# Performance work log

Measured on AMD Instinct MI355X. Metric: run time of the kernel, lower is better.

Reference implementation:

```python
import jax, jax.numpy as jnp
import numpy as np


def setup_inputs() -> dict:
    key = jax.random.key(0)
    ks = jax.random.split(key, 6)
    B, N, F, H, E = 2, 50000, 64, 32, 800000
    x = jax.random.normal(ks[0], (B, N, F), dtype=jnp.float32)
    edge_index = jax.random.randint(ks[1], (2, E), 0, N, dtype=jnp.int64)
    h_cur = jax.random.normal(ks[2], (B, N, H), dtype=jnp.float32)
    c_cur = jax.random.normal(ks[3], (B, N, H), dtype=jnp.float32)
    W = jax.random.normal(ks[4], (F + H, 4 * H), dtype=jnp.float32) * (1.0 / np.sqrt(F + H))
    b = jax.random.normal(ks[5], (4 * H,), dtype=jnp.float32) * 0.01
    return {"x": x, "edge_index": edge_index, "h_cur": h_cur, "c_cur": c_cur, "W": W, "b": b}


def reference(x, edge_index, h_cur, c_cur, W, b):
    B, N, _ = x.shape
    H = h_cur.shape[-1]

    # --- GCNConv on concatenated [x, h] ---
    combined = jnp.concatenate([x, h_cur], axis=-1)          # [B, N, F+H]
    xw = jnp.einsum('bnf,fg->bng', combined, W)              # [B, N, 4H]

    # add self-loops
    loop = jnp.arange(N, dtype=edge_index.dtype)
    src = jnp.concatenate([edge_index[0], loop])             # [E+N]
    dst = jnp.concatenate([edge_index[1], loop])             # [E+N]

    # symmetric degree normalization: deg over target index (PyG gcn_norm)
    deg = jnp.zeros((N,), dtype=xw.dtype).at[dst].add(1.0)
    dinv = jnp.where(deg > 0, jax.lax.rsqrt(deg), 0.0)
    norm = dinv[src] * dinv[dst]                             # [E+N]

    # gather-scale-scatter aggregation
    msgs = xw[:, src, :] * norm[None, :, None]               # [B, E+N, 4H]
    agg = jnp.zeros((B, N, 4 * H), dtype=xw.dtype).at[:, dst, :].add(msgs)
    conv = agg + b                                           # [B, N, 4H]

    # --- LSTM gating ---
    cc_i, cc_f, cc_o, cc_g = jnp.split(conv, 4, axis=-1)
    i = jax.nn.sigmoid(cc_i)
    f = jax.nn.sigmoid(cc_f)
    o = jax.nn.sigmoid(cc_o)
    g = jnp.tanh(cc_g)
    c_next = f * c_cur + i * g
    h_next = o * jnp.tanh(c_next)
    return h_next, c_next
```

## Files before the change

### kernel.cpp

```cpp
#include <hip/hip_runtime.h>
#include <hip/hip_bf16.h>

constexpr int H_DIM = 32;
constexpr int KPAD  = 104;
constexpr int CAP   = 64;
constexpr int PCAP  = 5120;
constexpr int EPB   = 2048;

typedef __attribute__((ext_vector_type(8))) short bf16x8;
typedef __attribute__((ext_vector_type(4))) float f32x4;

static __device__ __forceinline__ unsigned short f2bf_bits(float v) {
    __hip_bfloat16 b = __float2bfloat16(v);
    return *reinterpret_cast<unsigned short*>(&b);
}
static __device__ __forceinline__ unsigned pack2(float a, float b) {
    return (unsigned)f2bf_bits(a) | ((unsigned)f2bf_bits(b) << 16);
}
static __device__ __forceinline__ float lo_f(unsigned u) { return __uint_as_float(u << 16); }
static __device__ __forceinline__ float hi_f(unsigned u) { return __uint_as_float(u & 0xffff0000u); }

static __device__ __forceinline__ void fma4p(const uint4 u, float d, float* a)
{
    a[0] = fmaf(lo_f(u.x), d, a[0]);
    a[4] = fmaf(hi_f(u.x), d, a[4]);
    a[1] = fmaf(lo_f(u.y), d, a[1]);
    a[5] = fmaf(hi_f(u.y), d, a[5]);
    a[2] = fmaf(lo_f(u.z), d, a[2]);
    a[6] = fmaf(hi_f(u.z), d, a[6]);
    a[3] = fmaf(lo_f(u.w), d, a[3]);
    a[7] = fmaf(hi_f(u.w), d, a[7]);
}

__global__ __launch_bounds__(256)
void prep_kernel(const float* __restrict__ W,
                 unsigned short* __restrict__ Wt,
                 unsigned* __restrict__ pcnt)
{
    int gt = blockIdx.x * 256 + threadIdx.x;
    if (gt < 256) pcnt[gt] = 0u;
    if (gt < 96 * 128) {
        int k = gt >> 7;
        int n = gt & 127;
        Wt[n * 96 + k] = f2bf_bits(W[gt]);
    }
}

__global__ __launch_bounds__(256)
void part_convert_kernel(const float* __restrict__ x,
                         const float* __restrict__ h,
                         const int* __restrict__ ei,
                         unsigned* __restrict__ pcnt,
                         unsigned* __restrict__ part_buf,
                         unsigned* __restrict__ z,
                         int N, int E, int partGrid)
{
    const int bi = blockIdx.x;
    if (bi < partGrid) {
        __shared__ unsigned hist[256], basep[256], loff[256];
        const int t = threadIdx.x;
        hist[t] = 0u;
        loff[t] = 0u;
        __syncthreads();

        unsigned pk[8];
        const int e0 = bi * EPB + t;
        #pragma unroll
        for (int j = 0; j < 8; ++j) {
            int e = e0 + 256 * j;
            unsigned u = 0xFFFFFFFFu;
            if (e < E) {
                int src = ei[e];
                int dst = ei[E + e];
                int p   = dst >> 8;
                u = (unsigned)src | ((unsigned)(dst & 255) << 16) | ((unsigned)p << 24);
                atomicAdd(&hist[p], 1u);
            }
            pk[j] = u;
        }
        __syncthreads();
        if (hist[t]) basep[t] = atomicAdd(&pcnt[t], hist[t]);
        __syncthreads();
        #pragma unroll
        for (int j = 0; j < 8; ++j) {
            unsigned u = pk[j];
            if (u != 0xFFFFFFFFu) {
                int p = (int)(u >> 24);
                unsigned l = atomicAdd(&loff[p], 1u);
                unsigned slot = basep[p] + l;
                if (slot < PCAP) part_buf[(long)p * PCAP + slot] = u & 0x00FFFFFFu;
            }
        }
        return;
    }

    long idx = (long)(bi - partGrid) * 256 + threadIdx.x;
    if (idx >= (long)N * 24) return;
    int n  = (int)(idx / 24);
    int ku = (int)(idx - (long)n * 24);
    int f0 = 4 * ku;
    float4 a, b;
    if (f0 < 64) {
        a = *reinterpret_cast<const float4*>(x + (long)n * 64 + f0);
        b = *reinterpret_cast<const float4*>(x + ((long)N + n) * 64 + f0);
    } else {
        a = *reinterpret_cast<const float4*>(h + (long)n * 32 + (f0 - 64));
        b = *reinterpret_cast<const float4*>(h + ((long)N + n) * 32 + (f0 - 64));
    }
    uint4 o;
    o.x = pack2(a.x, b.x);
    o.y = pack2(a.y, b.y);
    o.z = pack2(a.z, b.z);
    o.w = pack2(a.w, b.w);
    *reinterpret_cast<uint4*>(z + idx * 4) = o;
}

__global__ __launch_bounds__(256)
void bucket_build_kernel(const unsigned* __restrict__ pcnt,
                         const unsigned* __restrict__ part_buf,
                         unsigned* __restrict__ cnt,
                         unsigned short* __restrict__ bucket,
                         int N)
{
    __shared__ unsigned lcnt[256];
    __shared__ __align__(16) unsigned short lbuck[256 * CAP];
    const int p = blockIdx.x;
    const int t = threadIdx.x;
    lcnt[t] = 0u;
    __syncthreads();

    const int cp = (int)min(pcnt[p], (unsigned)PCAP);
    const unsigned* __restrict__ pb = part_buf + (long)p * PCAP;
    for (int i = t; i < cp; i += 256) {
        unsigned u = pb[i];
        int dl = (int)((u >> 16) & 0xFFu);
        unsigned pos = atomicAdd(&lcnt[dl], 1u);
        if (pos < CAP) lbuck[dl * CAP + pos] = (unsigned short)(u & 0xFFFFu);
    }
    __syncthreads();

    int n = p * 256 + t;
    if (n < N) cnt[n] = lcnt[t];
    #pragma unroll
    for (int j = 0; j < 8; ++j) {
        int idx = t + 256 * j;
        int row = idx >> 3, c = idx & 7;
        int nn = p * 256 + row;
        if (nn < N)
            *reinterpret_cast<uint4*>(bucket + (long)nn * CAP + 8 * c) =
                *reinterpret_cast<const uint4*>(&lbuck[row * CAP + 8 * c]);
    }
}

__global__ __launch_bounds__(256)
void gather_kernel(const unsigned* __restrict__ cnt,
                   const unsigned short* __restrict__ bucket,
                   const unsigned* __restrict__ z,
                   unsigned* __restrict__ aggz, int N)
{
    const int wid  = (int)(((long)blockIdx.x * 256 + threadIdx.x) >> 6);
    const int lane = threadIdx.x & 63;
    const int g    = lane >> 5;
    const int w    = lane & 31;
    const bool live = (wid < N);
    const int n = live ? wid : 0;

    const int dn = live ? min((int)cnt[n], CAP) : 0;
    const unsigned short* __restrict__ brow = bucket + (long)n * CAP;
    const unsigned* __restrict__ zw = z + 4 * w;

    float acc[8];
    #pragma unroll
    for (int j = 0; j < 8; ++j) acc[j] = 0.f;

    for (int base = 0; base < dn; base += 64) {
        int cnt64 = min(64, dn - base);
        int   s_reg = 0;
        float d_reg = 0.f;
        if (lane < cnt64) {
            s_reg = (int)brow[base + lane];
            d_reg = rsqrtf((float)cnt[s_reg] + 1.f);
        }
        for (int i = 0; i < cnt64; i += 8) {
            int i0 = i + g, i1 = i + 2 + g, i2 = i + 4 + g, i3 = i + 6 + g;
            int   s0 = __shfl(s_reg, i0);  float d0 = __shfl(d_reg, i0);
            int   s1 = __shfl(s_reg, i1);  float d1 = __shfl(d_reg, i1);
            int   s2 = __shfl(s_reg, i2);  float d2 = __shfl(d_reg, i2);
            int   s3 = __shfl(s_reg, i3);  float d3 = __shfl(d_reg, i3);
            if (i0 >= cnt64) d0 = 0.f;
            if (i1 >= cnt64) d1 = 0.f;
            if (i2 >= cnt64) d2 = 0.f;
            if (i3 >= cnt64) d3 = 0.f;
            uint4 u0 = make_uint4(0,0,0,0), u1 = u0, u2 = u0, u3 = u0;
            if (w < 24) {
                u0 = *reinterpret_cast<const uint4*>(zw + (long)s0 * 96);
                u1 = *reinterpret_cast<const uint4*>(zw + (long)s1 * 96);
                u2 = *reinterpret_cast<const uint4*>(zw + (long)s2 * 96);
                u3 = *reinterpret_cast<const uint4*>(zw + (long)s3 * 96);
            }
            fma4p(u0, d0, acc);
            fma4p(u1, d1, acc);
            fma4p(u2, d2, acc);
            fma4p(u3, d3, acc);
        }
    }

    #pragma unroll
    for (int j = 0; j < 8; ++j) acc[j] += __shfl_xor(acc[j], 32);

    if (live && g == 0 && w < 24) {
        float di  = rsqrtf((float)cnt[n] + 1.f);
        float di2 = di * di;
        uint4 us = *reinterpret_cast<const uint4*>(zw + (long)n * 96);
        uint4 o;
        o.x = pack2(fmaf(di, acc[0], di2 * lo_f(us.x)), fmaf(di, acc[4], di2 * hi_f(us.x)));
        o.y = pack2(fmaf(di, acc[1], di2 * lo_f(us.y)), fmaf(di, acc[5], di2 * hi_f(us.y)));
        o.z = pack2(fmaf(di, acc[2], di2 * lo_f(us.z)), fmaf(di, acc[6], di2 * hi_f(us.z)));
        o.w = pack2(fmaf(di, acc[3], di2 * lo_f(us.w)), fmaf(di, acc[7], di2 * hi_f(us.w)));
        *reinterpret_cast<uint4*>(aggz + (long)n * 96 + 4 * w) = o;
    }
}

__global__ __launch_bounds__(256)
void gemm_gates_kernel(const unsigned* __restrict__ aggz,
                       const unsigned short* __restrict__ Wt,
                       const float* __restrict__ bias,
                       const float* __restrict__ c_cur,
                       float* __restrict__ out,
                       int N)
{
    __shared__ __align__(16) unsigned short As[64 * KPAD];
    const int t  = threadIdx.x;
    const int n0 = blockIdx.x * 32;

    #pragma unroll
    for (int j = 0; j < 3; ++j) {
        int idx = t + 256 * j;
        int i   = idx / 24;
        int ku  = idx - 24 * i;
        int n   = n0 + i;
        uint4 u = make_uint4(0,0,0,0);
        if (n < N) u = *reinterpret_cast<const uint4*>(aggz + (long)n * 96 + 4 * ku);
        ushort4 lo, hi;
        lo.x = (unsigned short)u.x;  hi.x = (unsigned short)(u.x >> 16);
        lo.y = (unsigned short)u.y;  hi.y = (unsigned short)(u.y >> 16);
        lo.z = (unsigned short)u.z;  hi.z = (unsigned short)(u.z >> 16);
        lo.w = (unsigned short)u.w;  hi.w = (unsigned short)(u.w >> 16);
        *reinterpret_cast<ushort4*>(&As[i * KPAD + 4 * ku])        = lo;
        *reinterpret_cast<ushort4*>(&As[(32 + i) * KPAD + 4 * ku]) = hi;
    }
    __syncthreads();

    const int wv   = t >> 6;
    const int lane = t & 63;
    const int m    = lane & 15;
    const int q    = lane >> 4;

    f32x4 acc[8] = {};
    #pragma unroll
    for (int k0 = 0; k0 < 96; k0 += 32) {
        bf16x8 a = *reinterpret_cast<const bf16x8*>(&As[(wv * 16 + m) * KPAD + k0 + q * 8]);
        #pragma unroll
        for (int nt = 0; nt < 8; ++nt) {
            bf16x8 b = *reinterpret_cast<const bf16x8*>(&Wt[(nt * 16 + m) * 96 + k0 + q * 8]);
            acc[nt] = __builtin_amdgcn_mfma_f32_16x16x32_bf16(a, b, acc[nt], 0, 0, 0);
        }
    }

    const float bi0 = bias[m],       bi1 = bias[16 + m];
    const float bf0 = bias[32 + m],  bf1 = bias[48 + m];
    const float bo0 = bias[64 + m],  bo1 = bias[80 + m];
    const float bg0 = bias[96 + m],  bg1 = bias[112 + m];
    const long  co  = (long)2 * N * H_DIM;

    #pragma unroll
    for (int r = 0; r < 4; ++r) {
        int rr = wv * 16 + q * 4 + r;
        int b  = rr >> 5;
        int i  = rr & 31;
        int n  = n0 + i;
        if (n < N) {
            long base = ((long)b * N + n) * H_DIM;
            float c0 = c_cur[base + m];
            float c1 = c_cur[base + 16 + m];
            float ig0 = 1.f / (1.f + __expf(-(acc[0][r] + bi0)));
            float ig1 = 1.f / (1.f + __expf(-(acc[1][r] + bi1)));
            float fg0 = 1.f / (1.f + __expf(-(acc[2][r] + bf0)));
            float fg1 = 1.f / (1.f + __expf(-(acc[3][r] + bf1)));
            float og0 = 1.f / (1.f + __expf(-(acc[4][r] + bo0)));
            float og1 = 1.f / (1.f + __expf(-(acc[5][r] + bo1)));
            float gg0 = tanhf(acc[6][r] + bg0);
            float gg1 = tanhf(acc[7][r] + bg1);
            float cn0 = fmaf(fg0, c0, ig0 * gg0);
            float cn1 = fmaf(fg1, c1, ig1 * gg1);
            out[base + m]           = og0 * tanhf(cn0);
            out[base + 16 + m]      = og1 * tanhf(cn1);
            out[co + base + m]      = cn0;
            out[co + base + 16 + m] = cn1;
        }
    }
}

extern "C" void kernel_launch(void* const* d_in, const int* in_sizes, int n_in,
                              void* d_out, int out_size, void* d_ws, size_t ws_size,
                              hipStream_t stream)
{
    const float* x    = (const float*)d_in[0];
    const int*   ei   = (const int*)d_in[1];
    const float* h    = (const float*)d_in[2];
    const float* c    = (const float*)d_in[3];
    const float* W    = (const float*)d_in[4];
    const float* bias = (const float*)d_in[5];

    const int  E  = in_sizes[1] / 2;
    const long BN = (long)in_sizes[2] / H_DIM;
    const int  N  = (int)(BN / 2);
    const int  NP = (N + 255) >> 8;

    char* ws = (char*)d_ws;
    unsigned* z = (unsigned*)ws;
    size_t off = (size_t)N * 96 * sizeof(unsigned);
    unsigned* aggz = (unsigned*)(ws + off);  off += (size_t)N * 96 * sizeof(unsigned);
    unsigned* cnt  = (unsigned*)(ws + off);  off += (size_t)N * sizeof(unsigned);
    unsigned short* bucket = (unsigned short*)(ws + off); off += (size_t)N * CAP * sizeof(unsigned short);
    unsigned short* Wt = (unsigned short*)(ws + off);     off += 96 * 128 * sizeof(unsigned short);
    off = (off + 255) & ~(size_t)255;
    unsigned* pcnt = (unsigned*)(ws + off);  off += 256 * sizeof(unsigned);
    unsigned* part_buf = (unsigned*)(ws + off); off += (size_t)NP * PCAP * sizeof(unsigned);

    int prep_grid = (96 * 128 + 255) / 256;
    prep_kernel<<<prep_grid, 256, 0, stream>>>(W, Wt, pcnt);

    int partGrid = (E + EPB - 1) / EPB;
    int convGrid = (int)(((long)N * 24 + 255) / 256);
    part_convert_kernel<<<partGrid + convGrid, 256, 0, stream>>>(
        x, h, ei, pcnt, part_buf, z, N, E, partGrid);

    bucket_build_kernel<<<NP, 256, 0, stream>>>(pcnt, part_buf, cnt, bucket, N);

    int gGrid = (int)(((long)N * 64 + 255) / 256);
    gather_kernel<<<gGrid, 256, 0, stream>>>(cnt, bucket, z, aggz, N);

    int mGrid = (N + 31) / 32;
    gemm_gates_kernel<<<mGrid, 256, 0, stream>>>(aggz, Wt, bias, c, (float*)d_out, N);
}
```

Before: 187.6 us.

## Fuse gather into GEMM, drop global partition atomics, merge W prep into bucket build

The change restructures the pipeline from five kernels to three. Edge partitioning now writes into per-block fixed-size chunks with a byte count instead of taking global atomic offsets, which removes the pcnt reset and the prep kernel. The W transpose moves into extra blocks of the bucket-build kernel. The gather is fused into the GEMM/gates kernel: each wave aggregates 8 nodes straight into shared memory with 8 loads in flight, which removes the aggz round trip through global memory. In exchange, each GEMM block has less parallelism for the latency-bound gather, and bucket build must scan NB chunks per partition.

```diff
diff --git a/kernel.cpp b/kernel.cpp
--- a/kernel.cpp
+++ b/kernel.cpp
@@ -4,7 +4,7 @@
 constexpr int H_DIM = 32;
 constexpr int KPAD  = 104;
 constexpr int CAP   = 64;
-constexpr int PCAP  = 5120;
+constexpr int CHK   = 64;
 constexpr int EPB   = 2048;
 
 typedef __attribute__((ext_vector_type(8))) short bf16x8;
@@ -33,68 +33,40 @@
 }
 
 __global__ __launch_bounds__(256)
-void prep_kernel(const float* __restrict__ W,
-                 unsigned short* __restrict__ Wt,
-                 unsigned* __restrict__ pcnt)
-{
-    int gt = blockIdx.x * 256 + threadIdx.x;
-    if (gt < 256) pcnt[gt] = 0u;
-    if (gt < 96 * 128) {
-        int k = gt >> 7;
-        int n = gt & 127;
-        Wt[n * 96 + k] = f2bf_bits(W[gt]);
-    }
-}
-
-__global__ __launch_bounds__(256)
 void part_convert_kernel(const float* __restrict__ x,
                          const float* __restrict__ h,
                          const int* __restrict__ ei,
-                         unsigned* __restrict__ pcnt,
                          unsigned* __restrict__ part_buf,
+                         unsigned char* __restrict__ hcnt,
                          unsigned* __restrict__ z,
-                         int N, int E, int partGrid)
+                         int N, int E, int NB)
 {
     const int bi = blockIdx.x;
-    if (bi < partGrid) {
-        __shared__ unsigned hist[256], basep[256], loff[256];
-        const int t = threadIdx.x;
-        hist[t] = 0u;
+    const int t  = threadIdx.x;
+    if (bi < NB) {
+        __shared__ unsigned loff[256];
         loff[t] = 0u;
         __syncthreads();
-
-        unsigned pk[8];
         const int e0 = bi * EPB + t;
         #pragma unroll
         for (int j = 0; j < 8; ++j) {
             int e = e0 + 256 * j;
-            unsigned u = 0xFFFFFFFFu;
             if (e < E) {
                 int src = ei[e];
                 int dst = ei[E + e];
                 int p   = dst >> 8;
-                u = (unsigned)src | ((unsigned)(dst & 255) << 16) | ((unsigned)p << 24);
-                atomicAdd(&hist[p], 1u);
+                unsigned pos = atomicAdd(&loff[p], 1u);
+                if (pos < CHK)
+                    part_buf[((long)p * NB + bi) * CHK + pos] =
+                        (unsigned)src | ((unsigned)(dst & 255) << 16);
             }
-            pk[j] = u;
         }
         __syncthreads();
-        if (hist[t]) basep[t] = atomicAdd(&pcnt[t], hist[t]);
-        __syncthreads();
-        #pragma unroll
-        for (int j = 0; j < 8; ++j) {
-            unsigned u = pk[j];
-            if (u != 0xFFFFFFFFu) {
-                int p = (int)(u >> 24);
-                unsigned l = atomicAdd(&loff[p], 1u);
-                unsigned slot = basep[p] + l;
-                if (slot < PCAP) part_buf[(long)p * PCAP + slot] = u & 0x00FFFFFFu;
-            }
-        }
+        hcnt[bi * 256 + t] = (unsigned char)min(loff[t], (unsigned)CHK);
         return;
     }
 
-    long idx = (long)(bi - partGrid) * 256 + threadIdx.x;
+    long idx = (long)(bi - NB) * 256 + t;
     if (idx >= (long)N * 24) return;
     int n  = (int)(idx / 24);
     int ku = (int)(idx - (long)n * 24);
@@ -116,26 +88,47 @@
 }
 
 __global__ __launch_bounds__(256)
-void bucket_build_kernel(const unsigned* __restrict__ pcnt,
-                         const unsigned* __restrict__ part_buf,
-                         unsigned* __restrict__ cnt,
-                         unsigned short* __restrict__ bucket,
-                         int N)
-{
+void bucket_prep_kernel(const unsigned* __restrict__ part_buf,
+                        const unsigned char* __restrict__ hcnt,
+                        const float* __restrict__ W,
+                        unsigned short* __restrict__ Wt,
+                        unsigned* __restrict__ cnt,
+                        unsigned short* __restrict__ bucket,
+                        int N, int NB, int NPART)
+{
+    const int t = threadIdx.x;
+    if ((int)blockIdx.x >= NPART) {
+        int gt = ((int)blockIdx.x - NPART) * 256 + t;
+        if (gt < 96 * 128) {
+            int k = gt >> 7;
+            int n = gt & 127;
+            Wt[n * 96 + k] = f2bf_bits(W[gt]);
+        }
+        return;
+    }
+
     __shared__ unsigned lcnt[256];
     __shared__ __align__(16) unsigned short lbuck[256 * CAP];
     const int p = blockIdx.x;
-    const int t = threadIdx.x;
     lcnt[t] = 0u;
     __syncthreads();
 
-    const int cp = (int)min(pcnt[p], (unsigned)PCAP);
-    const unsigned* __restrict__ pb = part_buf + (long)p * PCAP;
-    for (int i = t; i < cp; i += 256) {
-        unsigned u = pb[i];
-        int dl = (int)((u >> 16) & 0xFFu);
-        unsigned pos = atomicAdd(&lcnt[dl], 1u);
-        if (pos < CAP) lbuck[dl * CAP + pos] = (unsigned short)(u & 0xFFFFu);
+    for (int c = t; c < NB; c += 256) {
+        int cc = (int)hcnt[c * 256 + p];
+        const unsigned* __restrict__ pb = part_buf + ((long)p * NB + c) * CHK;
+        for (int jj = 0; jj < cc; jj += 4) {
+            uint4 u4 = *reinterpret_cast<const uint4*>(pb + jj);
+            unsigned uu[4] = {u4.x, u4.y, u4.z, u4.w};
+            #pragma unroll
+            for (int q2 = 0; q2 < 4; ++q2) {
+                if (jj + q2 < cc) {
+                    unsigned u = uu[q2];
+                    int dl = (int)((u >> 16) & 0xFFu);
+                    unsigned pos = atomicAdd(&lcnt[dl], 1u);
+                    if (pos < CAP) lbuck[dl * CAP + pos] = (unsigned short)(u & 0xFFFFu);
+                }
+            }
+        }
     }
     __syncthreads();
 
@@ -153,108 +146,90 @@
 }
 
 __global__ __launch_bounds__(256)
-void gather_kernel(const unsigned* __restrict__ cnt,
-                   const unsigned short* __restrict__ bucket,
-                   const unsigned* __restrict__ z,
-                   unsigned* __restrict__ aggz, int N)
-{
-    const int wid  = (int)(((long)blockIdx.x * 256 + threadIdx.x) >> 6);
-    const int lane = threadIdx.x & 63;
+void gather_gemm_kernel(const unsigned* __restrict__ cnt,
+                        const unsigned short* __restrict__ bucket,
+                        const unsigned* __restrict__ z,
+                        const unsigned short* __restrict__ Wt,
+                        const float* __restrict__ bias,
+                        const float* __restrict__ c_cur,
+                        float* __restrict__ out,
+                        int N)
+{
+    __shared__ __align__(16) unsigned short As[64 * KPAD];
+    const int t    = threadIdx.x;
+    const int n0   = blockIdx.x * 32;
+    const int wv   = t >> 6;
+    const int lane = t & 63;
     const int g    = lane >> 5;
     const int w    = lane & 31;
-    const bool live = (wid < N);
-    const int n = live ? wid : 0;
-
-    const int dn = live ? min((int)cnt[n], CAP) : 0;
-    const unsigned short* __restrict__ brow = bucket + (long)n * CAP;
     const unsigned* __restrict__ zw = z + 4 * w;
 
-    float acc[8];
-    #pragma unroll
-    for (int j = 0; j < 8; ++j) acc[j] = 0.f;
-
-    for (int base = 0; base < dn; base += 64) {
-        int cnt64 = min(64, dn - base);
-        int   s_reg = 0;
-        float d_reg = 0.f;
-        if (lane < cnt64) {
-            s_reg = (int)brow[base + lane];
-            d_reg = rsqrtf((float)cnt[s_reg] + 1.f);
-        }
-        for (int i = 0; i < cnt64; i += 8) {
-            int i0 = i + g, i1 = i + 2 + g, i2 = i + 4 + g, i3 = i + 6 + g;
-            int   s0 = __shfl(s_reg, i0);  float d0 = __shfl(d_reg, i0);
-            int   s1 = __shfl(s_reg, i1);  float d1 = __shfl(d_reg, i1);
-            int   s2 = __shfl(s_reg, i2);  float d2 = __shfl(d_reg, i2);
-            int   s3 = __shfl(s_reg, i3);  float d3 = __shfl(d_reg, i3);
-            if (i0 >= cnt64) d0 = 0.f;
-            if (i1 >= cnt64) d1 = 0.f;
-            if (i2 >= cnt64) d2 = 0.f;
-            if (i3 >= cnt64) d3 = 0.f;
-            uint4 u0 = make_uint4(0,0,0,0), u1 = u0, u2 = u0, u3 = u0;
-            if (w < 24) {
-                u0 = *reinterpret_cast<const uint4*>(zw + (long)s0 * 96);
-                u1 = *reinterpret_cast<const uint4*>(zw + (long)s1 * 96);
-                u2 = *reinterpret_cast<const uint4*>(zw + (long)s2 * 96);
-                u3 = *reinterpret_cast<const uint4*>(zw + (long)s3 * 96);
+    for (int s = 0; s < 8; ++s) {
+        const int n    = n0 + wv * 8 + s;
+        const bool live = (n < N);
+        const int nn   = live ? n : 0;
+        const int dn   = live ? min((int)cnt[nn], CAP) : 0;
+        const unsigned short* __restrict__ brow = bucket + (long)nn * CAP;
+
+        float acc[8];
+        #pragma unroll
+        for (int j = 0; j < 8; ++j) acc[j] = 0.f;
+
+        for (int base = 0; base < dn; base += 64) {
+            int cnt64 = min(64, dn - base);
+            int   s_reg = 0;
+            float d_reg = 0.f;
+            if (lane < cnt64) {
+                s_reg = (int)brow[base + lane];
+                d_reg = rsqrtf((float)cnt[s_reg] + 1.f);
             }
-            fma4p(u0, d0, acc);
-            fma4p(u1, d1, acc);
-            fma4p(u2, d2, acc);
-            fma4p(u3, d3, acc);
-        }
-    }
-
-    #pragma unroll
-    for (int j = 0; j < 8; ++j) acc[j] += __shfl_xor(acc[j], 32);
-
-    if (live && g == 0 && w < 24) {
-        float di  = rsqrtf((float)cnt[n] + 1.f);
-        float di2 = di * di;
-        uint4 us = *reinterpret_cast<const uint4*>(zw + (long)n * 96);
-        uint4 o;
-        o.x = pack2(fmaf(di, acc[0], di2 * lo_f(us.x)), fmaf(di, acc[4], di2 * hi_f(us.x)));
-        o.y = pack2(fmaf(di, acc[1], di2 * lo_f(us.y)), fmaf(di, acc[5], di2 * hi_f(us.y)));
-        o.z = pack2(fmaf(di, acc[2], di2 * lo_f(us.z)), fmaf(di, acc[6], di2 * hi_f(us.z)));
-        o.w = pack2(fmaf(di, acc[3], di2 * lo_f(us.w)), fmaf(di, acc[7], di2 * hi_f(us.w)));
-        *reinterpret_cast<uint4*>(aggz + (long)n * 96 + 4 * w) = o;
-    }
-}
-
-__global__ __launch_bounds__(256)
-void gemm_gates_kernel(const unsigned* __restrict__ aggz,
-                       const unsigned short* __restrict__ Wt,
-                       const float* __restrict__ bias,
-                       const float* __restrict__ c_cur,
-                       float* __restrict__ out,
-                       int N)
-{
-    __shared__ __align__(16) unsigned short As[64 * KPAD];
-    const int t  = threadIdx.x;
-    const int n0 = blockIdx.x * 32;
-
-    #pragma unroll
-    for (int j = 0; j < 3; ++j) {
-        int idx = t + 256 * j;
-        int i   = idx / 24;
-        int ku  = idx - 24 * i;
-        int n   = n0 + i;
-        uint4 u = make_uint4(0,0,0,0);
-        if (n < N) u = *reinterpret_cast<const uint4*>(aggz + (long)n * 96 + 4 * ku);
-        ushort4 lo, hi;
-        lo.x = (unsigned short)u.x;  hi.x = (unsigned short)(u.x >> 16);
-        lo.y = (unsigned short)u.y;  hi.y = (unsigned short)(u.y >> 16);
-        lo.z = (unsigned short)u.z;  hi.z = (unsigned short)(u.z >> 16);
-        lo.w = (unsigned short)u.w;  hi.w = (unsigned short)(u.w >> 16);
-        *reinterpret_cast<ushort4*>(&As[i * KPAD + 4 * ku])        = lo;
-        *reinterpret_cast<ushort4*>(&As[(32 + i) * KPAD + 4 * ku]) = hi;
+            for (int i = 0; i < cnt64; i += 16) {
+                int ss[8]; float dd[8]; uint4 u[8];
+                #pragma unroll
+                for (int j = 0; j < 8; ++j) {
+                    int ij = i + 2 * j + g;
+                    ss[j] = __shfl(s_reg, ij);
+                    dd[j] = __shfl(d_reg, ij);
+                    if (ij >= cnt64) dd[j] = 0.f;
+                }
+                #pragma unroll
+                for (int j = 0; j < 8; ++j) {
+                    int ij = i + 2 * j + g;
+                    u[j] = make_uint4(0u, 0u, 0u, 0u);
+                    if (w < 24 && ij < cnt64)
+                        u[j] = *reinterpret_cast<const uint4*>(zw + (long)ss[j] * 96);
+                }
+                #pragma unroll
+                for (int j = 0; j < 8; ++j) fma4p(u[j], dd[j], acc);
+            }
+        }
+
+        #pragma unroll
+        for (int j = 0; j < 8; ++j) acc[j] += __shfl_xor(acc[j], 32);
+
+        if (live && g == 0 && w < 24) {
+            float di  = rsqrtf((float)cnt[nn] + 1.f);
+            float di2 = di * di;
+            uint4 us = *reinterpret_cast<const uint4*>(zw + (long)nn * 96);
+            float l0 = fmaf(di, acc[0], di2 * lo_f(us.x));
+            float l1 = fmaf(di, acc[1], di2 * lo_f(us.y));
+            float l2 = fmaf(di, acc[2], di2 * lo_f(us.z));
+            float l3 = fmaf(di, acc[3], di2 * lo_f(us.w));
+            float h0 = fmaf(di, acc[4], di2 * hi_f(us.x));
+            float h1 = fmaf(di, acc[5], di2 * hi_f(us.y));
+            float h2 = fmaf(di, acc[6], di2 * hi_f(us.z));
+            float h3 = fmaf(di, acc[7], di2 * hi_f(us.w));
+            int r0 = wv * 8 + s;
+            *reinterpret_cast<uint2*>(&As[r0 * KPAD + 4 * w]) =
+                make_uint2(pack2(l0, l1), pack2(l2, l3));
+            *reinterpret_cast<uint2*>(&As[(32 + r0) * KPAD + 4 * w]) =
+                make_uint2(pack2(h0, h1), pack2(h2, h3));
+        }
     }
     __syncthreads();
 
-    const int wv   = t >> 6;
-    const int lane = t & 63;
-    const int m    = lane & 15;
-    const int q    = lane >> 4;
+    const int m = lane & 15;
+    const int q = lane >> 4;
 
     f32x4 acc[8] = {};
     #pragma unroll
@@ -316,31 +291,26 @@
     const long BN = (long)in_sizes[2] / H_DIM;
     const int  N  = (int)(BN / 2);
     const int  NP = (N + 255) >> 8;
+    const int  NB = (E + EPB - 1) / EPB;
 
     char* ws = (char*)d_ws;
     unsigned* z = (unsigned*)ws;
     size_t off = (size_t)N * 96 * sizeof(unsigned);
-    unsigned* aggz = (unsigned*)(ws + off);  off += (size_t)N * 96 * sizeof(unsigned);
-    unsigned* cnt  = (unsigned*)(ws + off);  off += (size_t)N * sizeof(unsigned);
+    unsigned* cnt = (unsigned*)(ws + off);   off += (size_t)N * sizeof(unsigned);
     unsigned short* bucket = (unsigned short*)(ws + off); off += (size_t)N * CAP * sizeof(unsigned short);
     unsigned short* Wt = (unsigned short*)(ws + off);     off += 96 * 128 * sizeof(unsigned short);
     off = (off + 255) & ~(size_t)255;
-    unsigned* pcnt = (unsigned*)(ws + off);  off += 256 * sizeof(unsigned);
-    unsigned* part_buf = (unsigned*)(ws + off); off += (size_t)NP * PCAP * sizeof(unsigned);
-
-    int prep_grid = (96 * 128 + 255) / 256;
-    prep_kernel<<<prep_grid, 256, 0, stream>>>(W, Wt, pcnt);
-
-    int partGrid = (E + EPB - 1) / EPB;
+    unsigned* part_buf = (unsigned*)(ws + off); off += (size_t)NP * NB * CHK * sizeof(unsigned);
+    unsigned char* hcnt = (unsigned char*)(ws + off); off += (size_t)NB * 256;
+
     int convGrid = (int)(((long)N * 24 + 255) / 256);
-    part_convert_kernel<<<partGrid + convGrid, 256, 0, stream>>>(
-        x, h, ei, pcnt, part_buf, z, N, E, partGrid);
-
-    bucket_build_kernel<<<NP, 256, 0, stream>>>(pcnt, part_buf, cnt, bucket, N);
-
-    int gGrid = (int)(((long)N * 64 + 255) / 256);
-    gather_kernel<<<gGrid, 256, 0, stream>>>(cnt, bucket, z, aggz, N);
+    part_convert_kernel<<<NB + convGrid, 256, 0, stream>>>(
+        x, h, ei, part_buf, hcnt, z, N, E, NB);
+
+    bucket_prep_kernel<<<NP + 48, 256, 0, stream>>>(
+        part_buf, hcnt, W, Wt, cnt, bucket, N, NB, NP);
 
     int mGrid = (N + 31) / 32;
-    gemm_gates_kernel<<<mGrid, 256, 0, stream>>>(aggz, Wt, bias, c, (float*)d_out, N);
-}
+    gather_gemm_kernel<<<mGrid, 256, 0, stream>>>(
+        cnt, bucket, z, Wt, bias, c, (float*)d_out, N);
+}
```

After: 190.8 us. No clear change (+1.7%).
